# Performance work log

Measured on AMD Instinct MI355X. Metric: run time of the kernel, lower is better.

## Reference

```python
import jax, jax.numpy as jnp
import numpy as np

D_MODEL, N_HEAD, N_KV_HEAD, D_HEAD = 1024, 16, 4, 64


def rotate_half(x):
    x1, x2 = x[..., : x.shape[-1] // 2], x[..., x.shape[-1] // 2:]
    return jnp.concatenate((-x2, x1), axis=-1)


def rope_cos_sin(seq_len, dim, dtype=jnp.float32):
    inv_freq = 1.0 / (10000.0 ** (jnp.arange(0, dim, 2, dtype=jnp.float32) / dim))
    t = jnp.arange(seq_len, dtype=jnp.float32)
    freqs = jnp.einsum('i,j->ij', t, inv_freq)          # [S, dim/2]
    emb = jnp.concatenate((freqs, freqs), axis=-1)       # [S, dim]
    return jnp.cos(emb).astype(dtype), jnp.sin(emb).astype(dtype)


def setup_inputs() -> dict:
    key = jax.random.key(0)
    ks = jax.random.split(key, 5)
    B, S = 2, 2048
    scale = 0.02
    return {
        'x': jax.random.normal(ks[0], (B, S, D_MODEL), dtype=jnp.float32),
        'Wq': jax.random.normal(ks[1], (D_MODEL, N_HEAD * D_HEAD), dtype=jnp.float32) * scale,
        'Wk': jax.random.normal(ks[2], (D_MODEL, N_KV_HEAD * D_HEAD), dtype=jnp.float32) * scale,
        'Wv': jax.random.normal(ks[3], (D_MODEL, N_KV_HEAD * D_HEAD), dtype=jnp.float32) * scale,
        'Wo': jax.random.normal(ks[4], (N_HEAD * D_HEAD, D_MODEL), dtype=jnp.float32) * scale,
    }


def reference(x, Wq, Wk, Wv, Wo):
    B, S, _ = x.shape
    scale = 1.0 / np.sqrt(D_HEAD)
    # projections -> [B, H, S, Dh]
    q = (x @ Wq).reshape(B, S, N_HEAD, D_HEAD).transpose(0, 2, 1, 3)
    k = (x @ Wk).reshape(B, S, N_KV_HEAD, D_HEAD).transpose(0, 2, 1, 3)
    v = (x @ Wv).reshape(B, S, N_KV_HEAD, D_HEAD).transpose(0, 2, 1, 3)
    cos, sin = rope_cos_sin(S, D_HEAD, x.dtype)          # [S, Dh]
    q = q * cos + rotate_half(q) * sin
    k = k * cos + rotate_half(k) * sin
    rep = N_HEAD // N_KV_HEAD
    k = jnp.repeat(k, rep, axis=1)                       # [B, H, S, Dh]
    v = jnp.repeat(v, rep, axis=1)
    scores = jnp.einsum('bhqd,bhkd->bhqk', q, k) * scale # [B, H, S, S]
    causal = jnp.triu(jnp.ones((S, S), dtype=bool), k=1)
    scores = jnp.where(causal, -jnp.inf, scores)
    probs = jax.nn.softmax(scores, axis=-1)
    ctx = jnp.einsum('bhqk,bhkd->bhqd', probs, v)        # [B, H, S, Dh]
    ctx = ctx.transpose(0, 2, 1, 3).reshape(B, S, N_HEAD * D_HEAD)
    return ctx @ Wo
```

## Files before the change

kernel.cpp:

```cpp
#include <hip/hip_runtime.h>
#include <hip/hip_bf16.h>
#include <cstdint>
#include <math.h>

#define S_LEN 2048
#define DM 1024
#define NQKV 1536
#define MROWS 4096
#define BKT 64

typedef __attribute__((ext_vector_type(8))) short short8;
typedef __attribute__((ext_vector_type(4))) float f32x4;
typedef __attribute__((ext_vector_type(16))) float f32x16;

#define QFOLD 0.18033688011112042f

__device__ __forceinline__ short f2bf(float x) {
  union { float f; uint32_t u; } v; v.f = x;
  uint32_t r = (v.u + 0x7fffu + ((v.u >> 16) & 1u)) >> 16;
  return (short)(uint16_t)r;
}

__device__ __forceinline__ uint32_t pk2(float a, float b) {
  __hip_bfloat162 h = __float22bfloat162_rn(make_float2(a, b));
  union { __hip_bfloat162 h2; uint32_t u; } cv; cv.h2 = h;
  return cv.u;
}

__global__ void f32_to_bf16_vec(const float* __restrict__ in, short* __restrict__ out, int n4) {
  int i = blockIdx.x * blockDim.x + threadIdx.x;
  if (i < n4) {
    float4 v = ((const float4*)in)[i];
    short4 o;
    o.x = f2bf(v.x); o.y = f2bf(v.y); o.z = f2bf(v.z); o.w = f2bf(v.w);
    ((short4*)out)[i] = o;
  }
}

__global__ __launch_bounds__(256) void transpose_f32_bf16(const float* __restrict__ src,
    short* __restrict__ dst, int R, int C) {
  __shared__ short T[64 * 72];
  const int r0 = blockIdx.x * 64, c0 = blockIdx.y * 64;
  const int tid = threadIdx.x;
  #pragma unroll
  for (int i = 0; i < 4; ++i) {
    int chunk = tid + i * 256;
    int r = chunk >> 4, cc = (chunk & 15) * 4;
    float4 v = *(const float4*)&src[(size_t)(r0 + r) * C + c0 + cc];
    T[(cc + 0) * 72 + r] = f2bf(v.x);
    T[(cc + 1) * 72 + r] = f2bf(v.y);
    T[(cc + 2) * 72 + r] = f2bf(v.z);
    T[(cc + 3) * 72 + r] = f2bf(v.w);
  }
  __syncthreads();
  #pragma unroll
  for (int i = 0; i < 2; ++i) {
    int chunk = tid + i * 256;
    int rr = chunk >> 3, kk = (chunk & 7) * 8;
    *(uint4*)&dst[(size_t)(c0 + rr) * R + r0 + kk] = *(uint4*)&T[rr * 72 + kk];
  }
}

template<int BMT, int BNT>
__global__ __launch_bounds__(256) void gemm_bf16_t(const short* __restrict__ A,
    const short* __restrict__ BT, float* __restrict__ C, int M, int N, int K) {
  constexpr int MI = BMT / 32, NI = BNT / 32;
  __shared__ short As[BMT * BKT];
  __shared__ short Bs[BNT * BKT];
  const int tid = threadIdx.x;
  const int wave = tid >> 6, lane = tid & 63;
  const int quad = lane >> 4, l15 = lane & 15;
  const int wm = (wave >> 1) * (BMT / 2), wn = (wave & 1) * (BNT / 2);
  const int m0 = blockIdx.y * BMT, n0 = blockIdx.x * BNT;
  const int rA = wave * (BMT / 4) + (lane >> 3);
  const int rB = wave * (BNT / 4) + (lane >> 3);
  const int scol = (lane & 7) * 8;

  f32x4 acc[MI][NI] = {};

  for (int k0 = 0; k0 < K; k0 += BKT) {
    __syncthreads();
    #pragma unroll
    for (int j = 0; j < MI; ++j)
      __builtin_amdgcn_global_load_lds(
          (const __attribute__((address_space(1))) void*)&A[(size_t)(m0 + rA + j * 8) * K + k0 + scol],
          (__attribute__((address_space(3))) void*)&As[(wave * MI + j) * 512],
          16, 0, 0);
    #pragma unroll
    for (int j = 0; j < NI; ++j)
      __builtin_amdgcn_global_load_lds(
          (const __attribute__((address_space(1))) void*)&BT[(size_t)(n0 + rB + j * 8) * K + k0 + scol],
          (__attribute__((address_space(3))) void*)&Bs[(wave * NI + j) * 512],
          16, 0, 0);
    __syncthreads();
    #pragma unroll
    for (int ks = 0; ks < 2; ++ks) {
      short8 af[MI], bfr[NI];
      #pragma unroll
      for (int mi = 0; mi < MI; ++mi)
        af[mi] = *(const short8*)&As[(wm + mi*16 + l15)*BKT + ks*32 + quad*8];
      #pragma unroll
      for (int ni = 0; ni < NI; ++ni)
        bfr[ni] = *(const short8*)&Bs[(wn + ni*16 + l15)*BKT + ks*32 + quad*8];
      #pragma unroll
      for (int mi = 0; mi < MI; ++mi)
        #pragma unroll
        for (int ni = 0; ni < NI; ++ni)
          acc[mi][ni] = __builtin_amdgcn_mfma_f32_16x16x32_bf16(af[mi], bfr[ni], acc[mi][ni], 0, 0, 0);
    }
  }
  #pragma unroll
  for (int mi = 0; mi < MI; ++mi)
    #pragma unroll
    for (int ni = 0; ni < NI; ++ni)
      #pragma unroll
      for (int r = 0; r < 4; ++r)
        C[(size_t)(m0 + wm + mi*16 + quad*4 + r)*N + (n0 + wn + ni*16 + l15)] = acc[mi][ni][r];
}

__global__ void rope_kernel(const float* __restrict__ qkv, short* __restrict__ Qb,
                            short* __restrict__ Kb, short* __restrict__ Vb) {
  __shared__ float csn[64];
  const int row = blockIdx.x;
  const int s = row & (S_LEN - 1);
  const int tid = threadIdx.x;
  const float* rp = qkv + (size_t)row * NQKV;
  if (tid < 32) {
    float inv = exp2f(-(float)tid * 0.41524101186092029f);
    float ang = (float)s * inv;
    csn[tid] = cosf(ang);
    csn[tid + 32] = sinf(ang);
  }
  __syncthreads();
  #pragma unroll
  for (int i = 0; i < 2; ++i) {
    int p = tid + i * 256;
    int hh = p >> 5, j = p & 31;
    float cs = csn[j], sn = csn[j + 32];
    float x1 = rp[hh*64 + j], x2 = rp[hh*64 + j + 32];
    Qb[(size_t)row*1024 + hh*64 + j]      = f2bf((x1*cs - x2*sn) * QFOLD);
    Qb[(size_t)row*1024 + hh*64 + j + 32] = f2bf((x2*cs + x1*sn) * QFOLD);
  }
  if (tid < 128) {
    int hh = tid >> 5, j = tid & 31;
    float cs = csn[j], sn = csn[j + 32];
    float x1 = rp[1024 + hh*64 + j], x2 = rp[1024 + hh*64 + j + 32];
    const int sw = (s & 7) << 3;
    Kb[(size_t)row*256 + hh*64 + (j ^ sw)]        = f2bf(x1*cs - x2*sn);
    Kb[(size_t)row*256 + hh*64 + ((j + 32) ^ sw)] = f2bf(x2*cs + x1*sn);
  }
  Vb[(size_t)row*256 + tid] = f2bf(rp[1280 + tid]);
}

__global__ __launch_bounds__(256) void transpose_v(const short* __restrict__ Vb,
                                                   short* __restrict__ Vt) {
  __shared__ short T[64 * 72];
  const int s0 = blockIdx.x * 64;
  const int bh = blockIdx.y;
  const int b = bh >> 2, kvh = bh & 3;
  const int tid = threadIdx.x;
  #pragma unroll
  for (int i = 0; i < 2; ++i) {
    int chunk = tid + i * 256;
    int r = chunk >> 3, c = (chunk & 7) * 8;
    short8 v = *(const short8*)&Vb[(size_t)(b*S_LEN + s0 + r)*256 + kvh*64 + c];
    #pragma unroll
    for (int t = 0; t < 8; ++t) T[(c + t) * 72 + r] = v[t];
  }
  __syncthreads();
  #pragma unroll
  for (int i = 0; i < 2; ++i) {
    int chunk = tid + i * 256;
    int rr = chunk >> 3, kk = (chunk & 7) * 8;
    *(uint4*)&Vt[(size_t)(bh*64 + rr)*S_LEN + s0 + (kk ^ ((rr & 7) << 3))] = *(uint4*)&T[rr * 72 + kk];
  }
}

__global__ __launch_bounds__(512, 4) void fattn9(const short* __restrict__ Qb,
    const short* __restrict__ Kb, const short* __restrict__ Vt, short* __restrict__ Ctx) {
  __shared__ short SMEM[32768];
  const int idx = blockIdx.x;
  const int pi  = idx & 15;
  const int h   = (idx >> 4) & 15;
  const int b   = idx >> 8;
  const int kvh = h >> 2;
  const int tid = threadIdx.x, wav = tid >> 6, lane = tid & 63;
  const int l31 = lane & 31, hi = lane >> 5;
  const int qs = wav & 1, g = wav >> 1;
  const int sx = (l31 & 7) << 3;
  const size_t qbase  = (size_t)b * S_LEN * 1024;
  const size_t kbase  = (size_t)b * S_LEN * 256;
  const size_t vtbase = (size_t)(b * 4 + kvh) * 64 * S_LEN;

  const short* kptr = Kb + kbase + (size_t)(wav * 16 + (lane >> 3)) * 256 + kvh * 64 + (lane & 7) * 8;
  const short* vptr = Vt + vtbase + (size_t)(wav * 8 + (lane >> 4)) * 2048 + (lane & 15) * 8;

#define STAGE(bi, k0s) do { \
    const short* kp_ = kptr + (size_t)(k0s) * 256; \
    const short* vp_ = vptr + (k0s); \
    short* kd_ = &SMEM[(bi) * 8192 + wav * 1024]; \
    short* vd_ = &SMEM[16384 + (bi) * 8192 + wav * 1024]; \
    _Pragma("unroll") \
    for (int i_ = 0; i_ < 2; ++i_) { \
      __builtin_amdgcn_global_load_lds((const __attribute__((address_space(1))) void*)(kp_ + i_ * 2048), \
          (__attribute__((address_space(3))) void*)(kd_ + i_ * 512), 16, 0, 0); \
      __builtin_amdgcn_global_load_lds((const __attribute__((address_space(1))) void*)(vp_ + i_ * 8192), \
          (__attribute__((address_space(3))) void*)(vd_ + i_ * 512), 16, 0, 0); \
    } \
  } while (0)

  for (int half = 0; half < 2; ++half) {
    const int jt = half ? (31 - pi) : pi;
    const int q0 = jt * 64;
    const int ntiles = (jt >> 1) + 1;
    const int qg = q0 + qs * 32 + l31;

    short8 qf[4];
    {
      const short* qp = &Qb[qbase + (size_t)qg * 1024 + h * 64 + hi * 8];
      #pragma unroll
      for (int ks = 0; ks < 4; ++ks) qf[ks] = *(const short8*)(qp + ks * 16);
    }

    f32x16 O0 = {}, O1 = {};
    float la0 = 0.f, la1 = 0.f, la2 = 0.f, la3 = 0.f;

    STAGE(0, 0);
    __syncthreads();

    for (int t = 0; t < ntiles; ++t) {
      const int cur = t & 1;
      const int k0 = t * 128;
      if (t + 1 < ntiles) STAGE((t + 1) & 1, (t + 1) * 128);

      const short* ks_ = &SMEM[cur * 8192];
      const short* vs_ = &SMEM[16384 + cur * 8192];

      f32x16 sc;
      __builtin_amdgcn_s_setprio(1);
      {
        const int r = g * 32 + l31;
        f32x16 a = {};
        #pragma unroll
        for (int ks2 = 0; ks2 < 4; ++ks2) {
          short8 kf = *(const short8*)&ks_[r * 64 + ((ks2 * 16 + hi * 8) ^ sx)];
          a = __builtin_amdgcn_mfma_f32_32x32x16_bf16(kf, qf[ks2], a, 0, 0, 0);
        }
        sc = a;
      }
      __builtin_amdgcn_s_setprio(0);

      if (t == ntiles - 1) {
        #pragma unroll
        for (int r = 0; r < 16; ++r) {
          const int kvg = k0 + g * 32 + (r & 3) + 8 * (r >> 2) + 4 * hi;
          if (kvg > qg) sc[r] = -1e30f;
        }
      }

      short8 af[2];
      {
        #pragma unroll
        for (int r = 0; r < 16; ++r) sc[r] = exp2f(sc[r]);
        la0 += (sc[0] + sc[1]) + (sc[2] + sc[3]);
        la1 += (sc[4] + sc[5]) + (sc[6] + sc[7]);
        la2 += (sc[8] + sc[9]) + (sc[10] + sc[11]);
        la3 += (sc[12] + sc[13]) + (sc[14] + sc[15]);
        #pragma unroll
        for (int st = 0; st < 2; ++st) {
          uint32_t x0 = pk2(sc[st * 8 + 0], sc[st * 8 + 1]);
          uint32_t x1 = pk2(sc[st * 8 + 2], sc[st * 8 + 3]);
          uint32_t x2 = pk2(sc[st * 8 + 4], sc[st * 8 + 5]);
          uint32_t x3 = pk2(sc[st * 8 + 6], sc[st * 8 + 7]);
          asm("v_permlane32_swap_b32 %0, %1" : "+v"(x0), "+v"(x2));
          asm("v_permlane32_swap_b32 %0, %1" : "+v"(x1), "+v"(x3));
          union { short8 s8; uint32_t u[4]; } cv;
          cv.u[0] = x0; cv.u[1] = x1; cv.u[2] = x2; cv.u[3] = x3;
          af[st] = cv.s8;
        }
      }

      __builtin_amdgcn_s_setprio(1);
      #pragma unroll
      for (int s = 0; s < 2; ++s) {
        const int co = g * 32 + s * 16 + hi * 8;
        short8 bv0 = *(const short8*)&vs_[l31 * 128 + (co ^ sx)];
        O0 = __builtin_amdgcn_mfma_f32_32x32x16_bf16(af[s], bv0, O0, 0, 0, 0);
        short8 bv1 = *(const short8*)&vs_[(32 + l31) * 128 + (co ^ sx)];
        O1 = __builtin_amdgcn_mfma_f32_32x32x16_bf16(af[s], bv1, O1, 0, 0, 0);
      }
      __builtin_amdgcn_s_setprio(0);

      __syncthreads();
    }

    float ll = (la0 + la1) + (la2 + la3);
    ll += __shfl_xor(ll, 32, 64);

    float* Os = (float*)SMEM;
    float* Ls = (float*)SMEM + 2 * 3 * 64 * 33;
    if (g > 0) {
      float* op = &Os[((qs * 3 + (g - 1)) * 64 + lane) * 33];
      #pragma unroll
      for (int r = 0; r < 16; ++r) { op[r] = O0[r]; op[16 + r] = O1[r]; }
      Ls[(qs * 3 + (g - 1)) * 64 + lane] = ll;
    }
    __syncthreads();
    if (g == 0) {
      #pragma unroll
      for (int src = 0; src < 3; ++src) {
        const float* op = &Os[((qs * 3 + src) * 64 + lane) * 33];
        #pragma unroll
        for (int r = 0; r < 16; ++r) { O0[r] += op[r]; O1[r] += op[16 + r]; }
        ll += Ls[(qs * 3 + src) * 64 + lane];
      }
      const float inv = 1.0f / ll;
      #pragma unroll
      for (int r = 0; r < 16; ++r) {
        const int crow = (r & 3) + 8 * (r >> 2) + 4 * hi;
        const float invr = __shfl(inv, crow, 64);
        const size_t o = qbase + (size_t)(q0 + qs * 32 + crow) * 1024 + h * 64;
        Ctx[o + l31]      = f2bf(O0[r] * invr);
        Ctx[o + 32 + l31] = f2bf(O1[r] * invr);
      }
    }
    __syncthreads();
  }
#undef STAGE
}

extern "C" void kernel_launch(void* const* d_in, const int* in_sizes, int n_in,
                              void* d_out, int out_size, void* d_ws, size_t ws_size,
                              hipStream_t stream) {
  const float* x  = (const float*)d_in[0];
  const float* Wq = (const float*)d_in[1];
  const float* Wk = (const float*)d_in[2];
  const float* Wv = (const float*)d_in[3];
  const float* Wo = (const float*)d_in[4];
  float* out = (float*)d_out;

  char* w = (char*)d_ws;
  short* Xb    = (short*)w;  w += (size_t)MROWS * DM * 2;
  short* WcatT = (short*)w;  w += (size_t)NQKV * DM * 2;
  short* WoT   = (short*)w;  w += (size_t)DM * DM * 2;
  float* QKVf  = (float*)w;  w += (size_t)MROWS * NQKV * 4;
  short* Qbuf  = (short*)w;  w += (size_t)MROWS * DM * 2;
  short* Kbuf  = (short*)w;  w += (size_t)MROWS * 256 * 2;
  short* Vbuf  = (short*)w;  w += (size_t)MROWS * 256 * 2;
  short* Vt    = (short*)w;  w += (size_t)8 * 64 * S_LEN * 2;
  short* Ctx   = (short*)QKVf;

  f32_to_bf16_vec<<<dim3(4096), dim3(256), 0, stream>>>(x, Xb, MROWS * DM / 4);
  transpose_f32_bf16<<<dim3(16, 16), dim3(256), 0, stream>>>(Wq, WcatT, 1024, 1024);
  transpose_f32_bf16<<<dim3(16, 4),  dim3(256), 0, stream>>>(Wk, WcatT + (size_t)1024*1024, 1024, 256);
  transpose_f32_bf16<<<dim3(16, 4),  dim3(256), 0, stream>>>(Wv, WcatT + (size_t)1280*1024, 1024, 256);
  transpose_f32_bf16<<<dim3(16, 16), dim3(256), 0, stream>>>(Wo, WoT, 1024, 1024);

  gemm_bf16_t<64,128><<<dim3(NQKV / 128, MROWS / 64), dim3(256), 0, stream>>>(Xb, WcatT, QKVf, MROWS, NQKV, DM);
  rope_kernel<<<dim3(MROWS), dim3(256), 0, stream>>>(QKVf, Qbuf, Kbuf, Vbuf);
  transpose_v<<<dim3(32, 8), dim3(256), 0, stream>>>(Vbuf, Vt);
  fattn9<<<dim3(512), dim3(512), 0, stream>>>(Qbuf, Kbuf, Vt, Ctx);
  gemm_bf16_t<64,128><<<dim3(DM / 128, MROWS / 64), dim3(256), 0, stream>>>(Ctx, WoT, out, MROWS, DM, DM);
}
```

Baseline: 185.3 us.

## Fuse prep kernels and restructure attention into 4-stage pipelined 256-thread blocks

Merges the x conversion and four weight-transpose launches into one prep kernel to cut launch overhead. The attention kernel drops from 8 to 4 waves per block and from 128-key to 64-key tiles. It gains a 4-deep LDS ring with explicit vmcnt waits and a single barrier per tile in place of double buffering with two barriers. This reduces cross-wave reduction work and sync cost but gives fewer waves per block for latency hiding and twice as many loop iterations.

```diff
diff --git a/kernel.cpp b/kernel.cpp
--- a/kernel.cpp
+++ b/kernel.cpp
@@ -27,21 +27,27 @@
   return cv.u;
 }
 
-__global__ void f32_to_bf16_vec(const float* __restrict__ in, short* __restrict__ out, int n4) {
-  int i = blockIdx.x * blockDim.x + threadIdx.x;
-  if (i < n4) {
-    float4 v = ((const float4*)in)[i];
+__global__ __launch_bounds__(256) void prep(const float* __restrict__ x,
+    const float* __restrict__ Wq, const float* __restrict__ Wk,
+    const float* __restrict__ Wv, const float* __restrict__ Wo,
+    short* __restrict__ Xb, short* __restrict__ WcatT, short* __restrict__ WoT) {
+  __shared__ short T[64 * 72];
+  const int bb = blockIdx.x;
+  const int tid = threadIdx.x;
+  if (bb < 4096) {
+    const int i = bb * 256 + tid;
+    float4 v = ((const float4*)x)[i];
     short4 o;
     o.x = f2bf(v.x); o.y = f2bf(v.y); o.z = f2bf(v.z); o.w = f2bf(v.w);
-    ((short4*)out)[i] = o;
-  }
-}
-
-__global__ __launch_bounds__(256) void transpose_f32_bf16(const float* __restrict__ src,
-    short* __restrict__ dst, int R, int C) {
-  __shared__ short T[64 * 72];
-  const int r0 = blockIdx.x * 64, c0 = blockIdx.y * 64;
-  const int tid = threadIdx.x;
+    ((short4*)Xb)[i] = o;
+    return;
+  }
+  const float* src; short* dst; int R, C, t2 = bb - 4096;
+  if (t2 < 256)      { src = Wq; dst = WcatT;                        R = 1024; C = 1024; }
+  else if (t2 < 320) { t2 -= 256; src = Wk; dst = WcatT + (size_t)1024*1024; R = 1024; C = 256; }
+  else if (t2 < 384) { t2 -= 320; src = Wv; dst = WcatT + (size_t)1280*1024; R = 1024; C = 256; }
+  else               { t2 -= 384; src = Wo; dst = WoT;               R = 1024; C = 1024; }
+  const int r0 = (t2 & 15) * 64, c0 = (t2 >> 4) * 64;
   #pragma unroll
   for (int i = 0; i < 4; ++i) {
     int chunk = tid + i * 256;
@@ -176,7 +182,7 @@
   }
 }
 
-__global__ __launch_bounds__(512, 4) void fattn9(const short* __restrict__ Qb,
+__global__ __launch_bounds__(256, 2) void fattn10(const short* __restrict__ Qb,
     const short* __restrict__ Kb, const short* __restrict__ Vt, short* __restrict__ Ctx) {
   __shared__ short SMEM[32768];
   const int idx = blockIdx.x;
@@ -193,18 +199,19 @@
   const size_t vtbase = (size_t)(b * 4 + kvh) * 64 * S_LEN;
 
   const short* kptr = Kb + kbase + (size_t)(wav * 16 + (lane >> 3)) * 256 + kvh * 64 + (lane & 7) * 8;
-  const short* vptr = Vt + vtbase + (size_t)(wav * 8 + (lane >> 4)) * 2048 + (lane & 15) * 8;
-
-#define STAGE(bi, k0s) do { \
-    const short* kp_ = kptr + (size_t)(k0s) * 256; \
-    const short* vp_ = vptr + (k0s); \
-    short* kd_ = &SMEM[(bi) * 8192 + wav * 1024]; \
-    short* vd_ = &SMEM[16384 + (bi) * 8192 + wav * 1024]; \
+  const short* vptr = Vt + vtbase + (size_t)(wav * 16 + (lane >> 3)) * 2048 + (lane & 7) * 8;
+
+#define STAGE(u) do { \
+    const int bi_ = (u) & 3; \
+    const short* kp_ = kptr + (size_t)(u) * 16384; \
+    const short* vp_ = vptr + (u) * 64; \
+    short* kd_ = &SMEM[bi_ * 8192 + wav * 1024]; \
+    short* vd_ = &SMEM[bi_ * 8192 + 4096 + wav * 1024]; \
     _Pragma("unroll") \
     for (int i_ = 0; i_ < 2; ++i_) { \
       __builtin_amdgcn_global_load_lds((const __attribute__((address_space(1))) void*)(kp_ + i_ * 2048), \
           (__attribute__((address_space(3))) void*)(kd_ + i_ * 512), 16, 0, 0); \
-      __builtin_amdgcn_global_load_lds((const __attribute__((address_space(1))) void*)(vp_ + i_ * 8192), \
+      __builtin_amdgcn_global_load_lds((const __attribute__((address_space(1))) void*)(vp_ + i_ * 16384), \
           (__attribute__((address_space(3))) void*)(vd_ + i_ * 512), 16, 0, 0); \
     } \
   } while (0)
@@ -212,7 +219,7 @@
   for (int half = 0; half < 2; ++half) {
     const int jt = half ? (31 - pi) : pi;
     const int q0 = jt * 64;
-    const int ntiles = (jt >> 1) + 1;
+    const int ntiles = jt + 1;
     const int qg = q0 + qs * 32 + l31;
 
     short8 qf[4];
@@ -225,16 +232,22 @@
     f32x16 O0 = {}, O1 = {};
     float la0 = 0.f, la1 = 0.f, la2 = 0.f, la3 = 0.f;
 
-    STAGE(0, 0);
-    __syncthreads();
+    STAGE(0);
+    if (ntiles > 1) STAGE(1);
+    if (ntiles > 2) STAGE(2);
 
     for (int t = 0; t < ntiles; ++t) {
-      const int cur = t & 1;
-      const int k0 = t * 128;
-      if (t + 1 < ntiles) STAGE((t + 1) & 1, (t + 1) * 128);
-
-      const short* ks_ = &SMEM[cur * 8192];
-      const short* vs_ = &SMEM[16384 + cur * 8192];
+      const int k0 = t * 64;
+      const int rem = ntiles - 1 - t;
+      if (rem >= 2)      { asm volatile("s_waitcnt vmcnt(8)" ::: "memory"); }
+      else if (rem == 1) { asm volatile("s_waitcnt vmcnt(4)" ::: "memory"); }
+      else               { asm volatile("s_waitcnt vmcnt(0)" ::: "memory"); }
+      __builtin_amdgcn_sched_barrier(0);
+      __builtin_amdgcn_s_barrier();
+      if (t + 3 < ntiles) STAGE(t + 3);
+
+      const short* ks_ = &SMEM[(t & 3) * 8192];
+      const short* vs_ = &SMEM[(t & 3) * 8192 + 4096];
 
       f32x16 sc;
       __builtin_amdgcn_s_setprio(1);
@@ -282,38 +295,34 @@
 
       __builtin_amdgcn_s_setprio(1);
       #pragma unroll
-      for (int s = 0; s < 2; ++s) {
-        const int co = g * 32 + s * 16 + hi * 8;
-        short8 bv0 = *(const short8*)&vs_[l31 * 128 + (co ^ sx)];
-        O0 = __builtin_amdgcn_mfma_f32_32x32x16_bf16(af[s], bv0, O0, 0, 0, 0);
-        short8 bv1 = *(const short8*)&vs_[(32 + l31) * 128 + (co ^ sx)];
-        O1 = __builtin_amdgcn_mfma_f32_32x32x16_bf16(af[s], bv1, O1, 0, 0, 0);
+      for (int s2 = 0; s2 < 2; ++s2) {
+        const int co = g * 32 + s2 * 16 + hi * 8;
+        short8 bv0 = *(const short8*)&vs_[l31 * 64 + (co ^ sx)];
+        O0 = __builtin_amdgcn_mfma_f32_32x32x16_bf16(af[s2], bv0, O0, 0, 0, 0);
+        short8 bv1 = *(const short8*)&vs_[(32 + l31) * 64 + (co ^ sx)];
+        O1 = __builtin_amdgcn_mfma_f32_32x32x16_bf16(af[s2], bv1, O1, 0, 0, 0);
       }
       __builtin_amdgcn_s_setprio(0);
-
-      __syncthreads();
     }
 
     float ll = (la0 + la1) + (la2 + la3);
     ll += __shfl_xor(ll, 32, 64);
+    __syncthreads();
 
     float* Os = (float*)SMEM;
-    float* Ls = (float*)SMEM + 2 * 3 * 64 * 33;
-    if (g > 0) {
-      float* op = &Os[((qs * 3 + (g - 1)) * 64 + lane) * 33];
+    float* Ls = (float*)SMEM + 2 * 64 * 33;
+    if (g == 1) {
+      float* op = &Os[(qs * 64 + lane) * 33];
       #pragma unroll
       for (int r = 0; r < 16; ++r) { op[r] = O0[r]; op[16 + r] = O1[r]; }
-      Ls[(qs * 3 + (g - 1)) * 64 + lane] = ll;
+      Ls[qs * 64 + lane] = ll;
     }
     __syncthreads();
     if (g == 0) {
-      #pragma unroll
-      for (int src = 0; src < 3; ++src) {
-        const float* op = &Os[((qs * 3 + src) * 64 + lane) * 33];
-        #pragma unroll
-        for (int r = 0; r < 16; ++r) { O0[r] += op[r]; O1[r] += op[16 + r]; }
-        ll += Ls[(qs * 3 + src) * 64 + lane];
-      }
+      const float* op = &Os[(qs * 64 + lane) * 33];
+      ll += Ls[qs * 64 + lane];
+      #pragma unroll
+      for (int r = 0; r < 16; ++r) { O0[r] += op[r]; O1[r] += op[16 + r]; }
       const float inv = 1.0f / ll;
       #pragma unroll
       for (int r = 0; r < 16; ++r) {
@@ -350,15 +359,11 @@
   short* Vt    = (short*)w;  w += (size_t)8 * 64 * S_LEN * 2;
   short* Ctx   = (short*)QKVf;
 
-  f32_to_bf16_vec<<<dim3(4096), dim3(256), 0, stream>>>(x, Xb, MROWS * DM / 4);
-  transpose_f32_bf16<<<dim3(16, 16), dim3(256), 0, stream>>>(Wq, WcatT, 1024, 1024);
-  transpose_f32_bf16<<<dim3(16, 4),  dim3(256), 0, stream>>>(Wk, WcatT + (size_t)1024*1024, 1024, 256);
-  transpose_f32_bf16<<<dim3(16, 4),  dim3(256), 0, stream>>>(Wv, WcatT + (size_t)1280*1024, 1024, 256);
-  transpose_f32_bf16<<<dim3(16, 16), dim3(256), 0, stream>>>(Wo, WoT, 1024, 1024);
+  prep<<<dim3(4736), dim3(256), 0, stream>>>(x, Wq, Wk, Wv, Wo, Xb, WcatT, WoT);
 
   gemm_bf16_t<64,128><<<dim3(NQKV / 128, MROWS / 64), dim3(256), 0, stream>>>(Xb, WcatT, QKVf, MROWS, NQKV, DM);
   rope_kernel<<<dim3(MROWS), dim3(256), 0, stream>>>(QKVf, Qbuf, Kbuf, Vbuf);
   transpose_v<<<dim3(32, 8), dim3(256), 0, stream>>>(Vbuf, Vt);
-  fattn9<<<dim3(512), dim3(512), 0, stream>>>(Qbuf, Kbuf, Vt, Ctx);
+  fattn10<<<dim3(512), dim3(256), 0, stream>>>(Qbuf, Kbuf, Vt, Ctx);
   gemm_bf16_t<64,128><<<dim3(DM / 128, MROWS / 64), dim3(256), 0, stream>>>(Ctx, WoT, out, MROWS, DM, DM);
 }
```

Measured after the change: 178.4 us. 3.7% less time.
